# Optimization experiments

Measured on AMD Instinct MI355X. Metric: run time of the kernel, lower is better.

Reference implementation:

```python
import jax, jax.numpy as jnp
import numpy as np

MS_TOKEN_SIZE = (1, 2, 4, 8, 16)  # divisor scales -> 'area' == exact average pooling


def _area_down(x, ph, pw):
    # F.interpolate(mode='area') with divisor target sizes == block average pool
    B, C, H, W = x.shape
    return x.reshape(B, C, ph, H // ph, pw, W // pw).mean(axis=(3, 5))


def _bicubic_up(x, H, W):
    # F.interpolate(mode='bicubic', align_corners=False) ~ jax.image.resize 'cubic'
    B, C, h, w = x.shape
    return jax.image.resize(x, (B, C, H, W), method='cubic')


def setup_inputs() -> dict:
    key = jax.random.key(0)
    k1, k2 = jax.random.split(key)
    z_enc = jax.random.normal(k1, (64, 32, 16, 16), dtype=jnp.float32)
    emb_weight = jax.random.normal(k2, (4096, 32), dtype=jnp.float32) * 0.01
    return {"z_enc": z_enc, "emb_weight": emb_weight}


def reference(z_enc, emb_weight):
    # obtain_multiscale_quantized_feature: multiscale residual VQ.
    # phi is identity (not defined in the provided source).
    B, C, H, W = z_enc.shape
    levels = len(MS_TOKEN_SIZE)
    z_rest = jax.lax.stop_gradient(z_enc)  # z_enc.detach()
    z_dec = jnp.zeros_like(z_rest)
    w_ng = jax.lax.stop_gradient(emb_weight)  # .data in distance computation
    w_sq = jnp.sum(w_ng * w_ng, axis=1)  # [K]
    ret = []
    for level, pn in enumerate(MS_TOKEN_SIZE):
        ph = pw = pn
        zd = _area_down(z_rest, ph, pw) if level != levels - 1 else z_rest
        zflat = zd.transpose(0, 2, 3, 1).reshape(-1, C)  # [B*ph*pw, C]
        # ||z||^2 + ||e||^2 - 2 z.e^T
        dist = (jnp.sum(zflat * zflat, axis=1, keepdims=True) + w_sq
                - 2.0 * (zflat @ w_ng.T))  # [B*ph*pw, K]
        token = jnp.argmin(dist, axis=1).reshape(B, ph, pw)
        z_up = jnp.take(emb_weight, token, axis=0).transpose(0, 3, 1, 2)  # [B,C,ph,pw]
        if level != levels - 1:
            z_up = _bicubic_up(z_up, H, W)
        z_dec = z_dec + z_up
        z_rest = z_rest - jax.lax.stop_gradient(z_up)
        ret.append(z_dec)
    return jnp.stack(ret)  # [levels, B, C, H, W]
```

## Files before the change

### kernel.cpp

```cpp
#include <hip/hip_runtime.h>

#define NB 64
#define NC 32
#define PLANE 256
#define NK 4096

__device__ __forceinline__ float cubic_w(float x) {
    x = fabsf(x);
    if (x >= 2.f) return 0.f;
    if (x >= 1.f) return ((-0.5f * x + 2.5f) * x - 4.f) * x + 2.f;
    return ((1.5f * x - 2.5f) * x) * x + 1.f;
}

template <int PN>
__device__ __forceinline__ void taps(int o, float* w, int& i0, int& n) {
    float sf = (o + 0.5f) * ((float)PN / 16.f) - 0.5f;
    int lo = (int)floorf(sf) - 1;
    int hi = lo + 3;
    if (lo < 0) lo = 0;
    if (hi > PN - 1) hi = PN - 1;
    n = hi - lo + 1;
    i0 = lo;
    float tot = 0.f;
    for (int i = 0; i < n; i++) {
        float ww = cubic_w(sf - (float)(lo + i));
        w[i] = ww;
        tot += ww;
    }
    float inv = 1.f / tot;
    for (int i = 0; i < n; i++) w[i] *= inv;
}

#define FMA4(D, A, B)                                                          \
    D = __builtin_fmaf((A).x, (B).x, D); D = __builtin_fmaf((A).y, (B).y, D);  \
    D = __builtin_fmaf((A).z, (B).z, D); D = __builtin_fmaf((A).w, (B).w, D)
#define DOT32(D)                                                               \
    FMA4(D, z0, w0); FMA4(D, z1, w1); FMA4(D, z2, w2); FMA4(D, z3, w3);        \
    FMA4(D, z4, w4); FMA4(D, z5, w5); FMA4(D, z6, w6); FMA4(D, z7, w7)
#define DOT32_2(DA, DB)                                                        \
    FMA4(DA, a0, w0); FMA4(DB, b0, w0); FMA4(DA, a1, w1); FMA4(DB, b1, w1);    \
    FMA4(DA, a2, w2); FMA4(DB, b2, w2); FMA4(DA, a3, w3); FMA4(DB, b3, w3);    \
    FMA4(DA, a4, w4); FMA4(DB, b4, w4); FMA4(DA, a5, w5); FMA4(DB, b5, w5);    \
    FMA4(DA, a6, w6); FMA4(DB, b6, w6); FMA4(DA, a7, w7); FMA4(DB, b7, w7)

__device__ __forceinline__ float pairwise_zsq(float4 z0, float4 z1, float4 z2,
                                              float4 z3, float4 z4, float4 z5,
                                              float4 z6, float4 z7) {
#define SQ_(a) __fmul_rn((a), (a))
#define R4_(a, b, c, d) \
    __fadd_rn(__fadd_rn(__fadd_rn(SQ_(a), SQ_(b)), SQ_(c)), SQ_(d))
    float r0 = R4_(z0.x, z2.x, z4.x, z6.x);
    float r1 = R4_(z0.y, z2.y, z4.y, z6.y);
    float r2 = R4_(z0.z, z2.z, z4.z, z6.z);
    float r3 = R4_(z0.w, z2.w, z4.w, z6.w);
    float r4 = R4_(z1.x, z3.x, z5.x, z7.x);
    float r5 = R4_(z1.y, z3.y, z5.y, z7.y);
    float r6 = R4_(z1.z, z3.z, z5.z, z7.z);
    float r7 = R4_(z1.w, z3.w, z5.w, z7.w);
    return __fadd_rn(__fadd_rn(__fadd_rn(r0, r1), __fadd_rn(r2, r3)),
                     __fadd_rn(__fadd_rn(r4, r5), __fadd_rn(r6, r7)));
#undef R4_
#undef SQ_
}

__global__ void __launch_bounds__(256) init_kernel(
    const float* __restrict__ z_enc, const float* __restrict__ emb,
    float* __restrict__ zflat0, float* __restrict__ wsq) {
    int bc = blockIdx.x;
    int t = threadIdx.x;
    float v = z_enc[bc * PLANE + t];
    for (int o = 32; o > 0; o >>= 1) v += __shfl_down(v, o, 64);
    __shared__ float p[4];
    if ((t & 63) == 0) p[t >> 6] = v;
    __syncthreads();
    if (t == 0) zflat0[bc] = (p[0] + p[1] + p[2] + p[3]) * (1.f / 256.f);
    if (t < 64) {
        int k = 2 * bc + (t >> 5);
        int c = t & 31;
        float e = emb[k * 32 + c];
        float s = __fmul_rn(e, e);
        for (int o = 16; o > 0; o >>= 1) s += __shfl_down(s, o, 32);
        if (c == 0) wsq[k] = s;
    }
}

template <int CPK>
__global__ void __launch_bounds__(64, 4) part2_kernel(
    const float* __restrict__ zflat, const float* __restrict__ emb,
    const float* __restrict__ wsq, float* __restrict__ cand_d,
    int* __restrict__ cand_i, int T) {
    int tokA = blockIdx.x * 128 + threadIdx.x;
    int tokB = tokA + 64;
    int KS = gridDim.y;
    int k0 = blockIdx.y * CPK;
    const float4* za = (const float4*)(zflat + (size_t)tokA * 32);
    const float4* zb = (const float4*)(zflat + (size_t)tokB * 32);
    float4 a0 = za[0], a1 = za[1], a2 = za[2], a3 = za[3];
    float4 a4 = za[4], a5 = za[5], a6 = za[6], a7 = za[7];
    float4 b0 = zb[0], b1 = zb[1], b2 = zb[2], b3 = zb[3];
    float4 b4 = zb[4], b5 = zb[5], b6 = zb[6], b7 = zb[7];
    float zsqA = pairwise_zsq(a0, a1, a2, a3, a4, a5, a6, a7);
    float zsqB = pairwise_zsq(b0, b1, b2, b3, b4, b5, b6, b7);

    float bestA = 1e30f, bestB = 1e30f;
    int biA = 0, biB = 0;
#pragma unroll 2
    for (int k = k0; k < k0 + CPK; k++) {
        const float4* wr = (const float4*)emb + (size_t)k * 8;
        float4 w0 = wr[0], w1 = wr[1], w2 = wr[2], w3 = wr[3];
        float4 w4 = wr[4], w5 = wr[5], w6 = wr[6], w7 = wr[7];
        float wk = wsq[k];
        float dotA = 0.f, dotB = 0.f;
        DOT32_2(dotA, dotB);
        float dA = __fsub_rn(__fadd_rn(zsqA, wk), __fmul_rn(2.f, dotA));
        float dB = __fsub_rn(__fadd_rn(zsqB, wk), __fmul_rn(2.f, dotB));
        if (dA < bestA) { bestA = dA; biA = k; }
        if (dB < bestB) { bestB = dB; biB = k; }
    }
    cand_d[(size_t)tokA * KS + blockIdx.y] = bestA;
    cand_i[(size_t)tokA * KS + blockIdx.y] = biA;
    cand_d[(size_t)tokB * KS + blockIdx.y] = bestB;
    cand_i[(size_t)tokB * KS + blockIdx.y] = biB;
}

template <int KPL>
__global__ void __launch_bounds__(64, 4) partk_kernel(
    const float* __restrict__ zflat, const float* __restrict__ emb,
    const float* __restrict__ wsq, float* __restrict__ cand_d,
    int* __restrict__ cand_i, int T) {
    int tok = blockIdx.x;
    int lane = threadIdx.x;
    int KS = gridDim.y;
    int kbase = blockIdx.y * (KPL * 64);
    const float4* zr = (const float4*)(zflat + (size_t)tok * 32);
    float4 z0 = zr[0], z1 = zr[1], z2 = zr[2], z3 = zr[3];
    float4 z4 = zr[4], z5 = zr[5], z6 = zr[6], z7 = zr[7];
    float zsq = pairwise_zsq(z0, z1, z2, z3, z4, z5, z6, z7);

    float best = 1e30f;
    int bi = 0;
#pragma unroll
    for (int j = 0; j < KPL; j++) {
        int k = kbase + j * 64 + lane;
        const float4* wr = (const float4*)emb + (size_t)k * 8;
        float4 w0 = wr[0], w1 = wr[1], w2 = wr[2], w3 = wr[3];
        float4 w4 = wr[4], w5 = wr[5], w6 = wr[6], w7 = wr[7];
        float dot = 0.f;
        DOT32(dot);
        float d = __fsub_rn(__fadd_rn(zsq, wsq[k]), __fmul_rn(2.f, dot));
        if (d < best) { best = d; bi = k; }
    }
    for (int off = 32; off > 0; off >>= 1) {
        float od = __shfl_down(best, off, 64);
        int oi = __shfl_down(bi, off, 64);
        if (od < best || (od == best && oi < bi)) { best = od; bi = oi; }
    }
    if (lane == 0) {
        cand_d[(size_t)tok * KS + blockIdx.y] = best;
        cand_i[(size_t)tok * KS + blockIdx.y] = bi;
    }
}

__global__ void __launch_bounds__(256) combine_wave(
    const float* __restrict__ cand_d, const int* __restrict__ cand_i,
    const float* __restrict__ emb, float* __restrict__ zq, int T, int KS) {
    int tok = (blockIdx.x * 256 + threadIdx.x) >> 6;
    int lane = threadIdx.x & 63;
    if (tok >= T) return;
    float best = 1e30f;
    int bi = 0x7fffffff;
    for (int s = lane; s < KS; s += 64) {
        float d = cand_d[(size_t)tok * KS + s];
        int i = cand_i[(size_t)tok * KS + s];
        if (d < best || (d == best && i < bi)) { best = d; bi = i; }
    }
    for (int off = 32; off > 0; off >>= 1) {
        float od = __shfl_down(best, off, 64);
        int oi = __shfl_down(bi, off, 64);
        if (od < best || (od == best && oi < bi)) { best = od; bi = oi; }
    }
    bi = __shfl(bi, 0, 64);
    if (lane < 8) {
        ((float4*)zq)[(size_t)tok * 8 + lane] =
            ((const float4*)emb)[(size_t)bi * 8 + lane];
    }
}

template <int PN, int PN_NEXT>
__global__ void __launch_bounds__(256) apply_kernel(
    const float* __restrict__ zrest_in, const float* __restrict__ zq,
    float* __restrict__ out_lvl, const float* __restrict__ out_prev,
    float* __restrict__ zrest_out, float* __restrict__ zflat_next) {
    __shared__ float rest[PLANE];
    int bc = blockIdx.x;
    int b = bc >> 5, c = bc & 31;
    int t = threadIdx.x;
    int h = t >> 4, w = t & 15;

    float zup;
    if constexpr (PN == 16) {
        zup = zq[(size_t)(((b * 16 + h) * 16 + w)) * 32 + c];
    } else {
        float wy[4], wx[4];
        int iy0, ny, jx0, nx;
        taps<PN>(h, wy, iy0, ny);
        taps<PN>(w, wx, jx0, nx);
        zup = 0.f;
        for (int e = 0; e < nx; e++) {
            float colacc = 0.f;
            for (int a = 0; a < ny; a++)
                colacc += wy[a] * zq[(size_t)((b * PN + iy0 + a) * PN + (jx0 + e)) * 32 + c];
            zup += wx[e] * colacc;
        }
    }
    int idx = bc * PLANE + t;
    float prev = out_prev ? out_prev[idx] : 0.f;
    out_lvl[idx] = __fadd_rn(prev, zup);

    if (zflat_next) {
        float rv = __fsub_rn(zrest_in[idx], zup);
        rest[t] = rv;
        if (zrest_out) zrest_out[idx] = rv;
        __syncthreads();
        constexpr int S = 16 / PN_NEXT;
        if (t < PN_NEXT * PN_NEXT) {
            int i = t / PN_NEXT, j = t % PN_NEXT;
            float s = 0.f;
            for (int di = 0; di < S; di++)
                for (int dj = 0; dj < S; dj++)
                    s = __fadd_rn(s, rest[(i * S + di) * 16 + (j * S + dj)]);
            zflat_next[(size_t)((b * PN_NEXT + i) * PN_NEXT + j) * 32 + c] =
                s * (1.f / (float)(S * S));
        }
    }
}

extern "C" void kernel_launch(void* const* d_in, const int* in_sizes, int n_in,
                              void* d_out, int out_size, void* d_ws, size_t ws_size,
                              hipStream_t stream) {
    const float* z_enc = (const float*)d_in[0];
    const float* emb   = (const float*)d_in[1];
    float* out = (float*)d_out;
    float* ws = (float*)d_ws;

    float* wsq    = ws;
    float* zflat  = wsq + NK;
    float* zq     = zflat + 524288;
    float* zrest  = zq + 524288;
    float* cand_d = zrest + 524288;
    int*   cand_i = (int*)(cand_d + 524288);

    const int LVL = NB * NC * PLANE;

    init_kernel<<<2048, 256, 0, stream>>>(z_enc, emb, zflat, wsq);

    partk_kernel<4><<<dim3(64, 16), 64, 0, stream>>>(zflat, emb, wsq, cand_d, cand_i, 64);
    combine_wave<<<16, 256, 0, stream>>>(cand_d, cand_i, emb, zq, 64, 16);
    apply_kernel<1, 2><<<2048, 256, 0, stream>>>(z_enc, zq, out, nullptr, zrest, zflat);

    partk_kernel<4><<<dim3(256, 16), 64, 0, stream>>>(zflat, emb, wsq, cand_d, cand_i, 256);
    combine_wave<<<64, 256, 0, stream>>>(cand_d, cand_i, emb, zq, 256, 16);
    apply_kernel<2, 4><<<2048, 256, 0, stream>>>(zrest, zq, out + LVL, out, zrest, zflat);

    part2_kernel<8><<<dim3(8, 512), 64, 0, stream>>>(zflat, emb, wsq, cand_d, cand_i, 1024);
    combine_wave<<<256, 256, 0, stream>>>(cand_d, cand_i, emb, zq, 1024, 512);
    apply_kernel<4, 8><<<2048, 256, 0, stream>>>(zrest, zq, out + 2 * LVL, out + LVL, zrest, zflat);

    part2_kernel<32><<<dim3(32, 128), 64, 0, stream>>>(zflat, emb, wsq, cand_d, cand_i, 4096);
    combine_wave<<<1024, 256, 0, stream>>>(cand_d, cand_i, emb, zq, 4096, 128);
    apply_kernel<8, 16><<<2048, 256, 0, stream>>>(zrest, zq, out + 3 * LVL, out + 2 * LVL, zrest, zflat);

    part2_kernel<128><<<dim3(128, 32), 64, 0, stream>>>(zflat, emb, wsq, cand_d, cand_i, 16384);
    combine_wave<<<4096, 256, 0, stream>>>(cand_d, cand_i, emb, zq, 16384, 32);
    apply_kernel<16, 16><<<2048, 256, 0, stream>>>(zrest, zq, out + 4 * LVL, out + 3 * LVL, nullptr, nullptr);
}
```

Baseline: 247.5 us.

## Stage codebook chunk in LDS and share it across four waves per block

The part2 distance kernel is replaced by a 256-thread version that cooperatively loads its codebook slice and squared norms into shared memory. Each of the four waves then reads codebook rows from LDS (broadcast reads) instead of each wave fetching them from global/L1. Token registers are pinned with empty asm to stop the compiler from rematerialising loads. The change adds a block barrier and LDS use, and the loop no longer carries an unroll pragma.

```diff
diff --git a/kernel.cpp b/kernel.cpp
--- a/kernel.cpp
+++ b/kernel.cpp
@@ -42,6 +42,8 @@
     FMA4(DA, a2, w2); FMA4(DB, b2, w2); FMA4(DA, a3, w3); FMA4(DB, b3, w3);    \
     FMA4(DA, a4, w4); FMA4(DB, b4, w4); FMA4(DA, a5, w5); FMA4(DB, b5, w5);    \
     FMA4(DA, a6, w6); FMA4(DB, b6, w6); FMA4(DA, a7, w7); FMA4(DB, b7, w7)
+
+#define PIN4(v) asm volatile("" : "+v"((v).x), "+v"((v).y), "+v"((v).z), "+v"((v).w))
 
 __device__ __forceinline__ float pairwise_zsq(float4 z0, float4 z1, float4 z2,
                                               float4 z3, float4 z4, float4 z5,
@@ -85,35 +87,52 @@
 }
 
 template <int CPK>
-__global__ void __launch_bounds__(64, 4) part2_kernel(
+__global__ void __launch_bounds__(256, 4) part_lds_kernel(
     const float* __restrict__ zflat, const float* __restrict__ emb,
     const float* __restrict__ wsq, float* __restrict__ cand_d,
     int* __restrict__ cand_i, int T) {
-    int tokA = blockIdx.x * 128 + threadIdx.x;
-    int tokB = tokA + 64;
+    __shared__ float4 wlds[CPK * 8];
+    __shared__ float wsqlds[CPK];
     int KS = gridDim.y;
     int k0 = blockIdx.y * CPK;
+    int t = threadIdx.x;
+
+    for (int i = t; i < CPK * 8; i += 256)
+        wlds[i] = ((const float4*)emb)[(size_t)k0 * 8 + i];
+    for (int i = t; i < CPK; i += 256)
+        wsqlds[i] = wsq[k0 + i];
+
+    int wave = t >> 6, lane = t & 63;
+    int tokA = (blockIdx.x * 4 + wave) * 128 + lane;
+    int tokB = tokA + 64;
     const float4* za = (const float4*)(zflat + (size_t)tokA * 32);
     const float4* zb = (const float4*)(zflat + (size_t)tokB * 32);
     float4 a0 = za[0], a1 = za[1], a2 = za[2], a3 = za[3];
     float4 a4 = za[4], a5 = za[5], a6 = za[6], a7 = za[7];
     float4 b0 = zb[0], b1 = zb[1], b2 = zb[2], b3 = zb[3];
     float4 b4 = zb[4], b5 = zb[5], b6 = zb[6], b7 = zb[7];
+    PIN4(a0); PIN4(a1); PIN4(a2); PIN4(a3);
+    PIN4(a4); PIN4(a5); PIN4(a6); PIN4(a7);
+    PIN4(b0); PIN4(b1); PIN4(b2); PIN4(b3);
+    PIN4(b4); PIN4(b5); PIN4(b6); PIN4(b7);
     float zsqA = pairwise_zsq(a0, a1, a2, a3, a4, a5, a6, a7);
     float zsqB = pairwise_zsq(b0, b1, b2, b3, b4, b5, b6, b7);
 
+    __syncthreads();
+
     float bestA = 1e30f, bestB = 1e30f;
     int biA = 0, biB = 0;
-#pragma unroll 2
-    for (int k = k0; k < k0 + CPK; k++) {
-        const float4* wr = (const float4*)emb + (size_t)k * 8;
-        float4 w0 = wr[0], w1 = wr[1], w2 = wr[2], w3 = wr[3];
-        float4 w4 = wr[4], w5 = wr[5], w6 = wr[6], w7 = wr[7];
-        float wk = wsq[k];
+    for (int kk = 0; kk < CPK; kk++) {
+        float4 w0 = wlds[kk * 8 + 0], w1 = wlds[kk * 8 + 1];
+        float4 w2 = wlds[kk * 8 + 2], w3 = wlds[kk * 8 + 3];
+        float4 w4 = wlds[kk * 8 + 4], w5 = wlds[kk * 8 + 5];
+        float4 w6 = wlds[kk * 8 + 6], w7 = wlds[kk * 8 + 7];
+        float wk = wsqlds[kk];
         float dotA = 0.f, dotB = 0.f;
         DOT32_2(dotA, dotB);
         float dA = __fsub_rn(__fadd_rn(zsqA, wk), __fmul_rn(2.f, dotA));
         float dB = __fsub_rn(__fadd_rn(zsqB, wk), __fmul_rn(2.f, dotB));
+        int k = k0 + kk;
         if (dA < bestA) { bestA = dA; biA = k; }
         if (dB < bestB) { bestB = dB; biB = k; }
     }
@@ -262,15 +281,15 @@
     combine_wave<<<64, 256, 0, stream>>>(cand_d, cand_i, emb, zq, 256, 16);
     apply_kernel<2, 4><<<2048, 256, 0, stream>>>(zrest, zq, out + LVL, out, zrest, zflat);
 
-    part2_kernel<8><<<dim3(8, 512), 64, 0, stream>>>(zflat, emb, wsq, cand_d, cand_i, 1024);
+    part_lds_kernel<8><<<dim3(2, 512), 256, 0, stream>>>(zflat, emb, wsq, cand_d, cand_i, 1024);
     combine_wave<<<256, 256, 0, stream>>>(cand_d, cand_i, emb, zq, 1024, 512);
     apply_kernel<4, 8><<<2048, 256, 0, stream>>>(zrest, zq, out + 2 * LVL, out + LVL, zrest, zflat);
 
-    part2_kernel<32><<<dim3(32, 128), 64, 0, stream>>>(zflat, emb, wsq, cand_d, cand_i, 4096);
+    part_lds_kernel<32><<<dim3(8, 128), 256, 0, stream>>>(zflat, emb, wsq, cand_d, cand_i, 4096);
     combine_wave<<<1024, 256, 0, stream>>>(cand_d, cand_i, emb, zq, 4096, 128);
     apply_kernel<8, 16><<<2048, 256, 0, stream>>>(zrest, zq, out + 3 * LVL, out + 2 * LVL, zrest, zflat);
 
-    part2_kernel<128><<<dim3(128, 32), 64, 0, stream>>>(zflat, emb, wsq, cand_d, cand_i, 16384);
+    part_lds_kernel<128><<<dim3(32, 32), 256, 0, stream>>>(zflat, emb, wsq, cand_d, cand_i, 16384);
     combine_wave<<<4096, 256, 0, stream>>>(cand_d, cand_i, emb, zq, 16384, 32);
     apply_kernel<16, 16><<<2048, 256, 0, stream>>>(zrest, zq, out + 4 * LVL, out + 3 * LVL, nullptr, nullptr);
 }
```

Measured after the change: 261.3 us. 5.6% more time.
